# Optimization experiments

Measured on AMD Instinct MI355X. Metric: run time of the kernel, lower is better.

The kernel has to match this reference:

```python
import jax, jax.numpy as jnp
import numpy as np

# ---- static ragged feature layout (from CTGAN metadata) ----
NUM_CLUSTERS = [10, 8, 10, 5, 10, 10, 7, 10, 10, 10]          # per numerical feature
NUM_CATEGORIES = [2, 5, 10, 3, 50, 4, 2, 8, 100, 6, 2, 3, 12, 5, 2, 30, 4, 9, 2, 7]
TAU = 0.2        # GumbelSoftmax temperature (teras default)
BN_EPS = 1e-3    # keras BatchNormalization default epsilon
LATENT_DIM = 128
BATCH = 65536

_seg, _alpha = [], []
_gid = 0
for c in NUM_CLUSTERS:
    _seg.append(_gid); _alpha.append(True); _gid += 1        # alpha scalar (tanh), own segment
    _seg += [_gid] * c; _alpha += [False] * c; _gid += 1     # beta cluster group (gumbel softmax)
for k in NUM_CATEGORIES:
    _seg += [_gid] * k; _alpha += [False] * k; _gid += 1     # categorical group (gumbel softmax)
SEG = jnp.asarray(np.array(_seg, dtype=np.int32))
ALPHA_MASK = jnp.asarray(np.array(_alpha, dtype=bool))
N_SEG = _gid
DATA_DIM = len(_seg)  # 366


def setup_inputs() -> dict:
    key = jax.random.key(0)
    ks = jax.random.split(key, 8)
    z = jax.random.normal(ks[0], (BATCH, LATENT_DIM), dtype=jnp.float32)
    # pre-sampled standard Gumbel noise for the gumbel-softmax groups
    u = jax.random.uniform(ks[1], (BATCH, DATA_DIM), dtype=jnp.float32, minval=1e-6, maxval=1.0 - 1e-6)
    g = -jnp.log(-jnp.log(u))
    def w(k, fi, fo):
        return jax.random.normal(k, (fi, fo), dtype=jnp.float32) * (1.0 / np.sqrt(fi))
    return {
        "z": z, "g": g,
        "W1": w(ks[2], LATENT_DIM, 256), "b1": jnp.zeros((256,), jnp.float32),
        "gamma1": jnp.ones((256,), jnp.float32), "beta1": jnp.zeros((256,), jnp.float32),
        "W2": w(ks[3], LATENT_DIM + 256, 256), "b2": jnp.zeros((256,), jnp.float32),
        "gamma2": jnp.ones((256,), jnp.float32), "beta2": jnp.zeros((256,), jnp.float32),
        "Wout": w(ks[4], LATENT_DIM + 512, DATA_DIM), "bout": jnp.zeros((DATA_DIM,), jnp.float32),
    }


def _bn_relu(h, gamma, beta):
    # training-mode batch norm (batch statistics), as used while training CTGAN
    mu = jnp.mean(h, axis=0)
    var = jnp.var(h, axis=0)
    return jax.nn.relu((h - mu) * jax.lax.rsqrt(var + BN_EPS) * gamma + beta)


def reference(z, g, W1, b1, gamma1, beta1, W2, b2, gamma2, beta2, Wout, bout):
    # CTGAN residual generator layers: out = concat([relu(bn(dense(x))), x])
    h1 = jnp.concatenate([_bn_relu(z @ W1 + b1, gamma1, beta1), z], axis=1)    # [B, 384]
    h2 = jnp.concatenate([_bn_relu(h1 @ W2 + b2, gamma2, beta2), h1], axis=1)  # [B, 640]
    logits = h2 @ Wout + bout                                                  # [B, 366]

    # ragged per-group gumbel-softmax: segment-wise stable softmax over columns
    zt = ((logits + g) / TAU).T                                   # [D, B]
    m = jax.ops.segment_max(zt, SEG, num_segments=N_SEG)          # [S, B]
    e = jnp.exp(zt - m[SEG])
    s = jax.ops.segment_sum(e, SEG, num_segments=N_SEG)
    soft = (e / s[SEG]).T                                         # [B, D]
    # alpha columns: tanh of raw logits; all other columns: group softmax
    return jnp.where(ALPHA_MASK[None, :], jnp.tanh(logits), soft)
```

## Files before the change

kernel.cpp:

```cpp
#include <hip/hip_runtime.h>

typedef _Float16 half_t;
typedef _Float16 half4 __attribute__((ext_vector_type(4)));
typedef _Float16 half8 __attribute__((ext_vector_type(8)));
typedef float f32x4 __attribute__((ext_vector_type(4)));

#define AS1 __attribute__((address_space(1)))
#define AS3 __attribute__((address_space(3)))

static constexpr int NBATCH = 65536;

__device__ __forceinline__ bool is_alpha(int c) {
  const unsigned long long AM0 =
      (1ull << 0) | (1ull << 11) | (1ull << 20) | (1ull << 31) | (1ull << 37) |
      (1ull << 48) | (1ull << 59);
  const unsigned long long AM1 = (1ull << 3) | (1ull << 14) | (1ull << 25);
  if (c >= 90) return false;
  return (((c < 64) ? (AM0 >> c) : (AM1 >> (c - 64))) & 1ull) != 0ull;
}

__device__ __forceinline__ half8 bn8(half8 x, half8 sc, half8 sh, half8 lo) {
  return __builtin_elementwise_max(x * sc + sh, lo);
}

__global__ __launch_bounds__(256) void k_cvtz(const float* __restrict__ z,
                                              half_t* __restrict__ dst) {
  size_t i = (size_t)blockIdx.x * 256 + threadIdx.x;
  int row = (int)(i >> 4), c8 = (int)(i & 15) << 3;
  const float* s = z + (size_t)row * 128 + c8;
  float4 v0 = *(const float4*)s;
  float4 v1 = *(const float4*)(s + 4);
  half8 h;
  h[0]=(half_t)v0.x; h[1]=(half_t)v0.y; h[2]=(half_t)v0.z; h[3]=(half_t)v0.w;
  h[4]=(half_t)v1.x; h[5]=(half_t)v1.y; h[6]=(half_t)v1.z; h[7]=(half_t)v1.w;
  *(half8*)(dst + (size_t)row * 640 + c8) = h;
}

__global__ __launch_bounds__(256) void k_transpose(const float* __restrict__ W,
                                                   half_t* __restrict__ Wt,
                                                   int K, int N, int total) {
  int i = blockIdx.x * 256 + threadIdx.x;
  if (i >= total) return;
  int n = i / K;
  int k = i - n * K;
  float v = (n < N) ? W[k * N + n] : 0.f;
  Wt[i] = (half_t)v;
}

__global__ void k_identtab(half_t* sc, half_t* sh, half_t* lo, int n) {
  int t = blockIdx.x * 128 + threadIdx.x;
  if (t < n) { sc[t] = (half_t)1.f; sh[t] = (half_t)0.f; lo[t] = (half_t)(-65504.f); }
}

template<bool STATS, bool TRANS, bool ALPHA>
__global__ __launch_bounds__(256) void k_gemm(
    const half_t* __restrict__ A, int lda, int K,
    const half_t* __restrict__ Bt,
    const float* __restrict__ bias,
    const half_t* __restrict__ tsc, const half_t* __restrict__ tsh,
    const half_t* __restrict__ tlo,
    half_t* __restrict__ o16, int ldo, int ncreal,
    float* __restrict__ ps, float* __restrict__ pq) {
  __shared__ __align__(16) char smem[32768];
  const int tid  = threadIdx.x;
  const int lane = tid & 63;
  const int w    = tid >> 6;
  const int wr   = w >> 1, wc = w & 1;
  const int ml   = lane & 15, g = lane >> 4;
  const int brow = blockIdx.x * 128;
  const int bcol = blockIdx.y * 128;
  const int sr  = lane >> 3;
  const int scg = (lane & 7) ^ sr;

  f32x4 acc[4][4];
#pragma unroll
  for (int i = 0; i < 4; i++)
#pragma unroll
    for (int j = 0; j < 4; j++) acc[i][j] = (f32x4){0.f, 0.f, 0.f, 0.f};

  const half_t* Abase = A  + (size_t)brow * lda;
  const half_t* Bbase = Bt + (size_t)bcol * K;
  const int nt = K >> 6;

  half_t* As = (half_t*)smem;
  half_t* Bs = (half_t*)(smem + 16384);

  for (int t = 0; t < nt; t++) {
    const int k0 = t * 64;
    half8 sc0, sh0, lo0, sc1, sh1, lo1;
    if (TRANS) {
      const int ka = k0 + g * 8, kb = k0 + 32 + g * 8;
      sc0 = *(const half8*)&tsc[ka]; sh0 = *(const half8*)&tsh[ka]; lo0 = *(const half8*)&tlo[ka];
      sc1 = *(const half8*)&tsc[kb]; sh1 = *(const half8*)&tsh[kb]; lo1 = *(const half8*)&tlo[kb];
    }
    if (t) __syncthreads();
#pragma unroll
    for (int it = 0; it < 4; it++) {
      int q = it * 4 + w;
      int r = q * 8 + sr;
      __builtin_amdgcn_global_load_lds(
          (AS1 const void*)(Abase + (size_t)r * lda + k0 + scg * 8),
          (AS3 void*)(As + q * 512), 16, 0, 0);
      __builtin_amdgcn_global_load_lds(
          (AS1 const void*)(Bbase + (size_t)r * K + k0 + scg * 8),
          (AS3 void*)(Bs + q * 512), 16, 0, 0);
    }
    __syncthreads();
#pragma unroll
    for (int t2 = 0; t2 < 2; t2++) {
      const int c4 = t2 * 4 + g;
      half8 af[4], bf[4];
#pragma unroll
      for (int fm = 0; fm < 4; fm++) {
        int row = wr * 64 + fm * 16 + ml;
        af[fm] = *(const half8*)((const char*)As + row * 128 + ((c4 ^ (row & 7)) << 4));
      }
      if (TRANS) {
        const half8 sc = t2 ? sc1 : sc0;
        const half8 sh = t2 ? sh1 : sh0;
        const half8 lo = t2 ? lo1 : lo0;
#pragma unroll
        for (int fm = 0; fm < 4; fm++) af[fm] = bn8(af[fm], sc, sh, lo);
      }
#pragma unroll
      for (int fn = 0; fn < 4; fn++) {
        int row = wc * 64 + fn * 16 + ml;
        bf[fn] = *(const half8*)((const char*)Bs + row * 128 + ((c4 ^ (row & 7)) << 4));
      }
#pragma unroll
      for (int fm = 0; fm < 4; fm++)
#pragma unroll
        for (int fn = 0; fn < 4; fn++)
          acc[fm][fn] = __builtin_amdgcn_mfma_f32_16x16x32_f16(af[fm], bf[fn], acc[fm][fn], 0, 0, 0);
    }
  }
  __syncthreads();

#pragma unroll
  for (int fn = 0; fn < 4; fn++) {
    int col  = wc * 64 + fn * 16 + ml;
    int gcol = bcol + col;
    float bz = (gcol < ncreal) ? bias[gcol] : 0.f;
    float s = 0.f, q = 0.f;
    const bool al = ALPHA && (gcol < 90) && is_alpha(gcol);
#pragma unroll
    for (int fm = 0; fm < 4; fm++)
#pragma unroll
      for (int rr = 0; rr < 4; rr++) {
        float v = acc[fm][fn][rr] + bz;
        if (STATS) { s += v; q += v * v; }
        if (al) v = tanhf(v);
        acc[fm][fn][rr] = v;
      }
    if (STATS) {
      s += __shfl_xor(s, 16, 64); s += __shfl_xor(s, 32, 64);
      q += __shfl_xor(q, 16, 64); q += __shfl_xor(q, 32, 64);
      if (g == 0) {
        ps[(size_t)gcol * 1024 + blockIdx.x * 2 + wr] = s;
        pq[(size_t)gcol * 1024 + blockIdx.x * 2 + wr] = q;
      }
    }
  }

  half_t* so = (half_t*)smem;
#pragma unroll
  for (int fn = 0; fn < 4; fn++)
#pragma unroll
    for (int fm = 0; fm < 4; fm++)
#pragma unroll
      for (int rr = 0; rr < 4; rr++)
        so[(wr * 64 + fm * 16 + g * 4 + rr) * 128 + wc * 64 + fn * 16 + ml] =
            (half_t)acc[fm][fn][rr];
  __syncthreads();
#pragma unroll
  for (int it = 0; it < 8; it++) {
    int r = it * 16 + (tid >> 4);
    int c = (tid & 15) * 8;
    *(half8*)(o16 + (size_t)(brow + r) * ldo + bcol + c) = *(const half8*)&so[r * 128 + c];
  }
}

__global__ __launch_bounds__(256) void k_bnfinal(
    const float* __restrict__ ps, const float* __restrict__ pq,
    const float* __restrict__ gamma, const float* __restrict__ beta,
    half_t* __restrict__ scA, half_t* __restrict__ shA, half_t* __restrict__ loA,
    half_t* __restrict__ scB, half_t* __restrict__ shB, half_t* __restrict__ loB) {
  int c = blockIdx.x, t = threadIdx.x;
  float s = 0.f, q = 0.f;
#pragma unroll
  for (int i = 0; i < 4; i++) {
    s += ps[(size_t)c * 1024 + t + i * 256];
    q += pq[(size_t)c * 1024 + t + i * 256];
  }
#pragma unroll
  for (int o = 1; o < 64; o <<= 1) { s += __shfl_xor(s, o, 64); q += __shfl_xor(q, o, 64); }
  __shared__ float ss[4], qq[4];
  if ((t & 63) == 0) { ss[t >> 6] = s; qq[t >> 6] = q; }
  __syncthreads();
  if (t == 0) {
    s = ss[0] + ss[1] + ss[2] + ss[3];
    q = qq[0] + qq[1] + qq[2] + qq[3];
    float mu   = s * (1.f / NBATCH);
    float var  = fmaxf(q * (1.f / NBATCH) - mu * mu, 0.f);
    float rstd = rsqrtf(var + 1e-3f);
    float a  = gamma[c] * rstd;
    float sh = beta[c] - mu * a;
    scA[c] = (half_t)a; shA[c] = (half_t)sh; loA[c] = (half_t)0.f;
    if (scB) { scB[c] = (half_t)a; shB[c] = (half_t)sh; loB[c] = (half_t)0.f; }
  }
}

template<int L>
__device__ __forceinline__ void seg_norm(float* __restrict__ zr, int S, int Lr) {
  float v[L];
#pragma unroll
  for (int j = 0; j < L; j++) v[j] = (j < Lr) ? zr[S + j] : -1e30f;
  float m = -1e30f;
#pragma unroll
  for (int j = 0; j < L; j++) m = fmaxf(m, v[j]);
  float s = 0.f;
#pragma unroll
  for (int j = 0; j < L; j++) { float e = __expf(v[j] - m); v[j] = e; s += e; }
  const float inv = 1.0f / s;
#pragma unroll
  for (int j = 0; j < L; j++)
    if (j < Lr) zr[S + j] = v[j] * inv;
}

template<int H>
__device__ __forceinline__ void seg_quad(float* __restrict__ zr, int base, int n) {
  float v[H];
#pragma unroll
  for (int j = 0; j < H; j++) v[j] = (j < n) ? zr[base + j] : -1e30f;
  float m = -1e30f;
#pragma unroll
  for (int j = 0; j < H; j++) m = fmaxf(m, v[j]);
  m = fmaxf(m, __shfl_xor(m, 1, 64));
  m = fmaxf(m, __shfl_xor(m, 2, 64));
  float s = 0.f;
#pragma unroll
  for (int j = 0; j < H; j++) { float e = __expf(v[j] - m); v[j] = e; s += e; }
  s += __shfl_xor(s, 1, 64);
  s += __shfl_xor(s, 2, 64);
  const float inv = 1.0f / s;
#pragma unroll
  for (int j = 0; j < H; j++)
    if (j < n) zr[base + j] = v[j] * inv;
}

__global__ __launch_bounds__(256, 6) void k_softmax(const half_t* __restrict__ lg,
                                                    const float* __restrict__ g,
                                                    float* __restrict__ out) {
  __shared__ float zb[16][373];
  const int tid  = threadIdx.x;
  const int row0 = blockIdx.x * 16;
  const size_t gbase = (size_t)row0 * 366;
  for (int i2 = tid; i2 < 16 * 183; i2 += 256) {
    int e0 = i2 * 2;
    int r = e0 / 366;
    int c = e0 - r * 366;
    const half_t* lp = lg + (size_t)(row0 + r) * 384 + c;
    float lx = (float)lp[0], ly = (float)lp[1];
    float2 gg = *(const float2*)(g + gbase + e0);
    zb[r][c]     = is_alpha(c)     ? lx : (lx + gg.x) * 5.0f;
    zb[r][c + 1] = is_alpha(c + 1) ? ly : (ly + gg.y) * 5.0f;
  }
  __syncthreads();
  {
    const int lane = tid & 63;
    const int w    = tid >> 6;
    const int quad = lane & 3;
    float* zr = &zb[lane >> 2][0];
    switch (w) {
      case 0:
        seg_quad<25>(zr, 184 + quad * 25, 25);
        break;
      case 1:
        seg_quad<13>(zr, 120 + quad * 13 - (quad >> 1) * (quad & 1), 13 - (quad >> 1));
        seg_quad<8>(zr, 314 + quad * 8 - (quad >> 1) * (quad & 1), 8 - (quad >> 1));
        break;
      case 2: {
        int s0 = (quad == 0) ? 295 : (quad == 1) ? 107 : (quad == 2) ? 38 : 68;
        int l0 = (quad == 0) ? 12 : 10;
        int s1 = (quad == 0) ? 1 : (quad == 1) ? 21 : (quad == 2) ? 49 : 79;
        int s2 = (quad == 0) ? 0 : (quad == 1) ? 100 : (quad == 2) ? 174 : 290;
        int l2 = (quad == 0) ? 0 : 2;
        seg_norm<12>(zr, s0, l0);
        seg_norm<10>(zr, s1, 10);
        seg_norm<2>(zr, s2, l2);
        break;
      }
      default: {
        int s0 = (quad == 0) ? 90 : (quad == 1) ? 12 : (quad == 2) ? 60 : 102;
        int l0 = (quad == 0) ? 10 : (quad == 1) ? 8 : (quad == 2) ? 7 : 5;
        int s1 = (quad == 0) ? 348 : (quad == 1) ? 176 : (quad == 2) ? 359 : 307;
        int l1 = (quad == 0) ? 9 : (quad == 1) ? 8 : (quad == 2) ? 7 : 5;
        int s2 = (quad == 0) ? 312 : (quad == 1) ? 284 : (quad == 2) ? 32 : 170;
        int l2 = (quad == 0) ? 2 : (quad == 1) ? 6 : (quad == 2) ? 5 : 4;
        int s3 = (quad == 0) ? 117 : (quad == 1) ? 357 : (quad == 2) ? 292 : 344;
        int l3 = (quad == 0) ? 3 : (quad == 1) ? 2 : (quad == 2) ? 3 : 4;
        seg_norm<10>(zr, s0, l0);
        seg_norm<9>(zr, s1, l1);
        seg_norm<6>(zr, s2, l2);
        seg_norm<4>(zr, s3, l3);
        break;
      }
    }
  }
  __syncthreads();
  for (int i2 = tid; i2 < 16 * 183; i2 += 256) {
    int e0 = i2 * 2;
    int r = e0 / 366;
    int c = e0 - r * 366;
    float2 v;
    v.x = zb[r][c];
    v.y = zb[r][c + 1];
    *(float2*)(out + gbase + e0) = v;
  }
}

extern "C" void kernel_launch(void* const* d_in, const int* in_sizes, int n_in,
                              void* d_out, int out_size, void* d_ws, size_t ws_size,
                              hipStream_t stream) {
  const float* z      = (const float*)d_in[0];
  const float* g      = (const float*)d_in[1];
  const float* W1     = (const float*)d_in[2];
  const float* b1     = (const float*)d_in[3];
  const float* gamma1 = (const float*)d_in[4];
  const float* beta1  = (const float*)d_in[5];
  const float* W2     = (const float*)d_in[6];
  const float* b2     = (const float*)d_in[7];
  const float* gamma2 = (const float*)d_in[8];
  const float* beta2  = (const float*)d_in[9];
  const float* Wout   = (const float*)d_in[10];
  const float* bout   = (const float*)d_in[11];
  float* out = (float*)d_out;
  char* ws = (char*)d_ws;

  size_t off = 0;
  half_t* act = (half_t*)(ws + off); off += (size_t)NBATCH * 640 * 2;
  half_t* lg  = (half_t*)(ws + off); off += (size_t)NBATCH * 384 * 2;
  half_t* W1t = (half_t*)(ws + off); off += (size_t)256 * 128 * 2;
  half_t* W2t = (half_t*)(ws + off); off += (size_t)256 * 384 * 2;
  half_t* Wot = (half_t*)(ws + off); off += (size_t)384 * 640 * 2;
  float*  ps  = (float*)(ws + off);  off += (size_t)256 * 1024 * 4;
  float*  pq  = (float*)(ws + off);  off += (size_t)256 * 1024 * 4;
  half_t* t2sc = (half_t*)(ws + off); off += 1024;
  half_t* t2sh = (half_t*)(ws + off); off += 1024;
  half_t* t2lo = (half_t*)(ws + off); off += 1024;
  half_t* t3sc = (half_t*)(ws + off); off += 2048;
  half_t* t3sh = (half_t*)(ws + off); off += 2048;
  half_t* t3lo = (half_t*)(ws + off); off += 2048;
  (void)ws_size; (void)in_sizes; (void)n_in; (void)out_size;

  k_cvtz<<<4096, 256, 0, stream>>>(z, act + 512);
  k_transpose<<<(256 * 128 + 255) / 256, 256, 0, stream>>>(W1, W1t, 128, 256, 256 * 128);
  k_transpose<<<(256 * 384 + 255) / 256, 256, 0, stream>>>(W2, W2t, 384, 256, 256 * 384);
  k_transpose<<<(384 * 640 + 255) / 256, 256, 0, stream>>>(Wout, Wot, 640, 366, 384 * 640);
  k_identtab<<<1, 128, 0, stream>>>(t2sc + 256, t2sh + 256, t2lo + 256, 128);
  k_identtab<<<1, 128, 0, stream>>>(t3sc + 512, t3sh + 512, t3lo + 512, 128);

  k_gemm<true, false, false><<<dim3(512, 2), 256, 0, stream>>>(
      act + 512, 640, 128, W1t, b1, nullptr, nullptr, nullptr,
      act + 256, 640, 256, ps, pq);
  k_bnfinal<<<256, 256, 0, stream>>>(ps, pq, gamma1, beta1,
                                     t2sc, t2sh, t2lo, t3sc + 256, t3sh + 256, t3lo + 256);

  k_gemm<true, true, false><<<dim3(512, 2), 256, 0, stream>>>(
      act + 256, 640, 384, W2t, b2, t2sc, t2sh, t2lo,
      act + 0, 640, 256, ps, pq);
  k_bnfinal<<<256, 256, 0, stream>>>(ps, pq, gamma2, beta2,
                                     t3sc, t3sh, t3lo, nullptr, nullptr, nullptr);

  k_gemm<false, true, true><<<dim3(512, 3), 256, 0, stream>>>(
      act, 640, 640, Wot, bout, t3sc, t3sh, t3lo,
      lg, 384, 366, nullptr, nullptr);

  k_softmax<<<NBATCH / 16, 256, 0, stream>>>(lg, g, out);
}
```

Baseline: 186.1 us.

## Double-buffer GEMM LDS tiles with BK=32 and stage BN tables in LDS

Reworks the GEMM main loop from single-buffered 64-wide K tiles into a double-buffered pipeline of 32-wide K tiles. The next tile's async global-to-LDS loads are issued before computing the current one, synchronised with vmcnt waits and raw barriers. The BN scale, shift and clamp tables are copied into LDS once instead of read from global each iteration, and the swizzle is changed for the narrower tile. This aims to hide global load latency behind MFMA work, at the cost of more barriers per K step and a little more LDS per block.

```diff
diff --git a/kernel.cpp b/kernel.cpp
--- a/kernel.cpp
+++ b/kernel.cpp
@@ -61,7 +61,7 @@
     const half_t* __restrict__ tlo,
     half_t* __restrict__ o16, int ldo, int ncreal,
     float* __restrict__ ps, float* __restrict__ pq) {
-  __shared__ __align__(16) char smem[32768];
+  __shared__ __align__(16) char smem[36864];
   const int tid  = threadIdx.x;
   const int lane = tid & 63;
   const int w    = tid >> 6;
@@ -69,8 +69,9 @@
   const int ml   = lane & 15, g = lane >> 4;
   const int brow = blockIdx.x * 128;
   const int bcol = blockIdx.y * 128;
-  const int sr  = lane >> 3;
-  const int scg = (lane & 7) ^ sr;
+  const int r4   = lane >> 2;
+  const int scg  = (lane & 3) ^ ((lane >> 3) & 3);
+  const int cl   = g ^ ((ml >> 1) & 3);
 
   f32x4 acc[4][4];
 #pragma unroll
@@ -80,60 +81,81 @@
 
   const half_t* Abase = A  + (size_t)brow * lda;
   const half_t* Bbase = Bt + (size_t)bcol * K;
-  const int nt = K >> 6;
-
-  half_t* As = (half_t*)smem;
-  half_t* Bs = (half_t*)(smem + 16384);
-
-  for (int t = 0; t < nt; t++) {
-    const int k0 = t * 64;
-    half8 sc0, sh0, lo0, sc1, sh1, lo1;
-    if (TRANS) {
-      const int ka = k0 + g * 8, kb = k0 + 32 + g * 8;
-      sc0 = *(const half8*)&tsc[ka]; sh0 = *(const half8*)&tsh[ka]; lo0 = *(const half8*)&tlo[ka];
-      sc1 = *(const half8*)&tsc[kb]; sh1 = *(const half8*)&tsh[kb]; lo1 = *(const half8*)&tlo[kb];
-    }
-    if (t) __syncthreads();
-#pragma unroll
-    for (int it = 0; it < 4; it++) {
+  const int nt = K >> 5;
+
+  auto stage = [&](int t, int p) {
+    const int k0 = t * 32;
+    char* As = smem + p * 16384;
+    char* Bs = smem + p * 16384 + 8192;
+#pragma unroll
+    for (int it = 0; it < 2; it++) {
       int q = it * 4 + w;
-      int r = q * 8 + sr;
+      int r = q * 16 + r4;
       __builtin_amdgcn_global_load_lds(
           (AS1 const void*)(Abase + (size_t)r * lda + k0 + scg * 8),
-          (AS3 void*)(As + q * 512), 16, 0, 0);
+          (AS3 void*)(As + q * 1024), 16, 0, 0);
       __builtin_amdgcn_global_load_lds(
           (AS1 const void*)(Bbase + (size_t)r * K + k0 + scg * 8),
-          (AS3 void*)(Bs + q * 512), 16, 0, 0);
-    }
-    __syncthreads();
-#pragma unroll
-    for (int t2 = 0; t2 < 2; t2++) {
-      const int c4 = t2 * 4 + g;
-      half8 af[4], bf[4];
-#pragma unroll
-      for (int fm = 0; fm < 4; fm++) {
-        int row = wr * 64 + fm * 16 + ml;
-        af[fm] = *(const half8*)((const char*)As + row * 128 + ((c4 ^ (row & 7)) << 4));
-      }
-      if (TRANS) {
-        const half8 sc = t2 ? sc1 : sc0;
-        const half8 sh = t2 ? sh1 : sh0;
-        const half8 lo = t2 ? lo1 : lo0;
-#pragma unroll
-        for (int fm = 0; fm < 4; fm++) af[fm] = bn8(af[fm], sc, sh, lo);
-      }
-#pragma unroll
-      for (int fn = 0; fn < 4; fn++) {
-        int row = wc * 64 + fn * 16 + ml;
-        bf[fn] = *(const half8*)((const char*)Bs + row * 128 + ((c4 ^ (row & 7)) << 4));
-      }
-#pragma unroll
-      for (int fm = 0; fm < 4; fm++)
-#pragma unroll
-        for (int fn = 0; fn < 4; fn++)
-          acc[fm][fn] = __builtin_amdgcn_mfma_f32_16x16x32_f16(af[fm], bf[fn], acc[fm][fn], 0, 0, 0);
-    }
-  }
+          (AS3 void*)(Bs + q * 1024), 16, 0, 0);
+    }
+  };
+
+  auto compute = [&](int t, int p) {
+    const char* As = smem + p * 16384;
+    const char* Bs = smem + p * 16384 + 8192;
+    half8 sc, sh, lo;
+    if (TRANS) {
+      const half_t* tb = (const half_t*)(smem + 32768);
+      int o = t * 32 + g * 8;
+      sc = *(const half8*)(tb + o);
+      sh = *(const half8*)(tb + 640 + o);
+      lo = *(const half8*)(tb + 1280 + o);
+    }
+    half8 af[4], bf[4];
+#pragma unroll
+    for (int fm = 0; fm < 4; fm++) {
+      int row = wr * 64 + fm * 16 + ml;
+      af[fm] = *(const half8*)(As + row * 64 + cl * 16);
+    }
+    if (TRANS) {
+#pragma unroll
+      for (int fm = 0; fm < 4; fm++) af[fm] = bn8(af[fm], sc, sh, lo);
+    }
+#pragma unroll
+    for (int fn = 0; fn < 4; fn++) {
+      int row = wc * 64 + fn * 16 + ml;
+      bf[fn] = *(const half8*)(Bs + row * 64 + cl * 16);
+    }
+#pragma unroll
+    for (int fm = 0; fm < 4; fm++)
+#pragma unroll
+      for (int fn = 0; fn < 4; fn++)
+        acc[fm][fn] = __builtin_amdgcn_mfma_f32_16x16x32_f16(af[fm], bf[fn], acc[fm][fn], 0, 0, 0);
+  };
+
+  if (TRANS) {
+    const int no = K >> 3;
+    for (int i = tid; i < 3 * no; i += 256) {
+      int a = i / no, pos = i - a * no;
+      const half_t* src = (a == 0 ? tsc : (a == 1 ? tsh : tlo)) + pos * 8;
+      *(half8*)(smem + 32768 + a * 1280 + pos * 16) = *(const half8*)src;
+    }
+  }
+  stage(0, 0);
+  asm volatile("s_waitcnt lgkmcnt(0)" ::: "memory");
+
+  int p = 0;
+  for (int t = 0; t < nt - 1; t++) {
+    stage(t + 1, p ^ 1);
+    asm volatile("s_waitcnt vmcnt(4)" ::: "memory");
+    __builtin_amdgcn_s_barrier();
+    compute(t, p);
+    __builtin_amdgcn_s_barrier();
+    p ^= 1;
+  }
+  asm volatile("s_waitcnt vmcnt(0)" ::: "memory");
+  __builtin_amdgcn_s_barrier();
+  compute(nt - 1, p);
   __syncthreads();
 
 #pragma unroll
```

Result: slower. 190.2 us (+2.2%).
